# Kernel optimization log

Hardware: AMD Instinct MI355X
Metric: run time of the kernel (lower is better)

Reference implementation:

```python
import jax, jax.numpy as jnp
import numpy as np

B, L, H, N = 8, 8192, 128, 32  # batch, seq_len, d_model, d_state//2 (complex)


def setup_inputs() -> dict:
    key = jax.random.key(0)
    ks = jax.random.split(key, 13)
    x = jax.random.normal(ks[0], (B, L, 2), dtype=jnp.float32)
    enc_w = jax.random.normal(ks[1], (2, H), dtype=jnp.float32) * (1.0 / np.sqrt(2.0))
    enc_b = jax.random.normal(ks[2], (H,), dtype=jnp.float32) * 0.01
    # S4D init: dt log-uniform in [1e-3, 1e-1], A = -0.5 + i*pi*n (S4D-Lin)
    u01 = jax.random.uniform(ks[3], (H,), dtype=jnp.float32)
    log_dt = u01 * (np.log(0.1) - np.log(0.001)) + np.log(0.001)
    log_A_real = jnp.full((H, N), np.log(0.5), dtype=jnp.float32)
    A_imag = jnp.broadcast_to(np.pi * jnp.arange(N, dtype=jnp.float32), (H, N)).copy()
    C_re = jax.random.normal(ks[4], (H, N), dtype=jnp.float32) * (0.5 ** 0.5)
    C_im = jax.random.normal(ks[5], (H, N), dtype=jnp.float32) * (0.5 ** 0.5)
    D = jax.random.normal(ks[6], (H,), dtype=jnp.float32)
    out_w = jax.random.normal(ks[7], (2 * H, H), dtype=jnp.float32) * (1.0 / np.sqrt(H))
    out_b = jax.random.normal(ks[8], (2 * H,), dtype=jnp.float32) * 0.01
    dec_w = jax.random.normal(ks[9], (H, 1), dtype=jnp.float32) * (1.0 / np.sqrt(H))
    dec_b = jax.random.normal(ks[10], (1,), dtype=jnp.float32) * 0.01
    return {"x": x, "enc_w": enc_w, "enc_b": enc_b, "log_dt": log_dt,
            "log_A_real": log_A_real, "A_imag": A_imag, "C_re": C_re,
            "C_im": C_im, "D": D, "out_w": out_w, "out_b": out_b,
            "dec_w": dec_w, "dec_b": dec_b}


def reference(x, enc_w, enc_b, log_dt, log_A_real, A_imag, C_re, C_im, D,
              out_w, out_b, dec_w, dec_b):
    # Encoder (B,L,2) -> (B,L,H), then transpose to channels-first (B,H,L)
    u = jnp.einsum('blc,ch->blh', x, enc_w) + enc_b
    u = jnp.swapaxes(u, -1, -2)  # (B,H,L)
    Lx = u.shape[-1]

    # --- S4D kernel (zero-order-hold discretization, diagonal A) ---
    dt = jnp.exp(log_dt)                      # (H,)
    A = -jnp.exp(log_A_real) + 1j * A_imag    # (H,N) complex
    C = C_re + 1j * C_im                      # (H,N)
    dtA = dt[:, None] * A                     # (H,N)
    K_coef = C * (jnp.exp(dtA) - 1.0) / A     # (H,N)
    # Vandermonde: exp(dtA * l), l = 0..L-1  -> (H,N,L)
    vand = jnp.exp(dtA[:, :, None] * jnp.arange(Lx, dtype=jnp.float32))
    K = 2.0 * jnp.einsum('hn,hnl->hl', K_coef, vand).real  # (H,L)

    # --- causal convolution via FFT (length 2L avoids circular wrap) ---
    n = 2 * Lx
    y = jnp.fft.irfft(jnp.fft.rfft(u, n) * jnp.fft.rfft(K, n), n)[..., :Lx]
    y = y + D[:, None] * u                    # skip connection

    # GELU -> pointwise GLU output projection (Conv1d(H, 2H, 1) + GLU)
    y = jax.nn.gelu(y)
    z = jnp.einsum('bhl,gh->bgl', y, out_w) + out_b[None, :, None]  # (B,2H,L)
    a, g = jnp.split(z, 2, axis=1)
    y = a * jax.nn.sigmoid(g)                 # (B,H,L)

    # Mean-pool over sequence, decode to scalar: (B,1)
    pooled = jnp.mean(y, axis=-1)             # (B,H)
    return pooled @ dec_w + dec_b
```

## Files before the change

### kernel.cpp

```cpp
#include <hip/hip_runtime.h>
#include <math.h>

#define B_ 8
#define L_ 8192
#define H_ 128
#define N_ 32
#define C_ 128
#define T_ 64


typedef _Float16 half8 __attribute__((ext_vector_type(8)));
typedef __attribute__((ext_vector_type(4))) float f32x4;

__device__ __forceinline__ float gelu_tanh(float y) {
    float t = 0.7978845608028654f * fmaf(0.044715f, y * y * y, y);
    float e = __expf(2.f * t);
    float th = 1.f - __fdividef(2.f, e + 1.f);
    return 0.5f * y * (1.f + th);
}
__device__ __forceinline__ unsigned short f2h(float f) {
    _Float16 h = (_Float16)f;
    return *(unsigned short*)&h;
}
__device__ __forceinline__ float h2f(unsigned short u) {
    return (float)(*(const _Float16*)&u);
}

__global__ __launch_bounds__(256) void k_prep(
    const float* __restrict__ log_dt, const float* __restrict__ log_A_real,
    const float* __restrict__ A_imag, const float* __restrict__ C_re,
    const float* __restrict__ C_im, const float* __restrict__ out_w,
    unsigned short* __restrict__ Wh, unsigned short* __restrict__ Kh,
    unsigned short* __restrict__ Ph, unsigned short* __restrict__ Vh)
{
    const int h = blockIdx.x;
    const int tid = threadIdx.x;
    __shared__ float2 wtab[65][N_];
    __shared__ float2 coefs[N_];
    __shared__ float Kd[64];

    float dt = expf(log_dt[h]);
#pragma unroll
    for (int it = 0; it < 9; ++it) {
        int idx = it * 256 + tid;
        if (idx < 65 * N_) {
            int d = idx >> 5, n = idx & 31;
            float Ar = -expf(log_A_real[h * N_ + n]);
            float Ai = A_imag[h * N_ + n];
            float ar = dt * Ar * (float)d, ai = dt * Ai * (float)d;
            float er = expf(ar);
            wtab[d][n] = make_float2(er * cosf(ai), er * sinf(ai));
        }
    }
    if (tid < N_) {
        int n = tid;
        float Ar = -expf(log_A_real[h * N_ + n]);
        float Ai = A_imag[h * N_ + n];
        float ar = dt * Ar, ai = dt * Ai;
        float er = expf(ar);
        float wr = er * cosf(ai), wi = er * sinf(ai);
        float inv = 1.f / (Ar * Ar + Ai * Ai);
        float numr = wr - 1.f, numi = wi;
        float qr = (numr * Ar + numi * Ai) * inv;
        float qi = (numi * Ar - numr * Ai) * inv;
        coefs[n] = make_float2(C_re[h * N_ + n] * qr - C_im[h * N_ + n] * qi,
                               C_re[h * N_ + n] * qi + C_im[h * N_ + n] * qr);
    }
    __syncthreads();
    if (tid < 64) {
        float s = 0.f;
#pragma unroll
        for (int n = 0; n < N_; ++n) {
            float2 cf = coefs[n]; float2 w = wtab[tid][n];
            s += cf.x * w.x - cf.y * w.y;
        }
        Kd[tid] = 2.f * s;
    }
    __syncthreads();
#pragma unroll
    for (int it = 0; it < 16; ++it) {
        int idx = it * 256 + tid;
        int t = idx >> 6, j = idx & 63;
        Kh[h * 4096 + idx] = f2h((t >= j) ? Kd[t - j] : 0.f);
    }
#pragma unroll
    for (int it = 0; it < 16; ++it) {
        int idx = it * 256 + tid;
        int t = idx >> 6, m = idx & 63, n = m & 31;
        float2 cf = coefs[n]; float2 w = wtab[t + 1][n];
        float re = cf.x * w.x - cf.y * w.y;
        float im = cf.x * w.y + cf.y * w.x;
        Ph[h * 4096 + idx] = f2h((m < 32) ? 2.f * re : -2.f * im);
    }
#pragma unroll
    for (int it = 0; it < 16; ++it) {
        int idx = it * 256 + tid;
        int m = idx >> 6, j = idx & 63, n = m & 31;
        float2 w = wtab[63 - j][n];
        Vh[h * 4096 + idx] = f2h((m < 32) ? w.x : w.y);
    }
    {
        int g = 2 * h + (tid >> 7), j = tid & 127;
        Wh[g * 128 + j] = f2h(out_w[g * 128 + j]);
    }
}

__global__ __launch_bounds__(256) void k_s4d(
    const float* __restrict__ x, const float* __restrict__ enc_w,
    const float* __restrict__ enc_b, const float* __restrict__ log_dt,
    const float* __restrict__ log_A_real, const float* __restrict__ A_imag,
    const float* __restrict__ Dp, const unsigned short* __restrict__ Kh,
    const unsigned short* __restrict__ Ph, const unsigned short* __restrict__ Vh,
    unsigned short* __restrict__ gy)
{
    const int bh = blockIdx.x;
    const int b = bh >> 7, h = bh & (H_ - 1);
    const int tid = threadIdx.x;
    const int lane = tid & 63, wq = tid >> 6;
    const int mrow = lane & 15, quad = lane >> 4;

    __shared__ unsigned short Ut[C_][72];
    __shared__ __align__(16) char scratch[18432];
    __shared__ float2 wTpow[7][N_];
    unsigned short* E16 = (unsigned short*)scratch;
    float2*         Sx  = (float2*)scratch;
    unsigned short* St  = (unsigned short*)scratch;

    if (tid < N_) {
        int idx = h * N_ + tid;
        float dt = expf(log_dt[h]);
        float Ar = -expf(log_A_real[idx]);
        float Ai = A_imag[idx];
        float ar = dt * Ar * (float)T_, ai = dt * Ai * (float)T_;
        float er = expf(ar);
        float pr = er * cosf(ai), pi = er * sinf(ai);
#pragma unroll
        for (int k = 0; k < 7; ++k) {
            wTpow[k][tid] = make_float2(pr, pi);
            float nr = pr * pr - pi * pi;
            pi = 2.f * pr * pi; pr = nr;
        }
    }

    const float ew0 = enc_w[h], ew1 = enc_w[H_ + h], eb = enc_b[h];
    {
        int c = tid >> 1, j0 = (tid & 1) * 32;
        const float4* xp = (const float4*)((const float2*)x + (size_t)b * L_
                                           + c * 64 + j0);
#pragma unroll
        for (int i = 0; i < 16; ++i) {
            float4 xv = xp[i];
            float u0 = fmaf(xv.x, ew0, fmaf(xv.y, ew1, eb));
            float u1 = fmaf(xv.z, ew0, fmaf(xv.w, ew1, eb));
            unsigned int pk = (unsigned)f2h(u0) | ((unsigned)f2h(u1) << 16);
            *(unsigned int*)&Ut[c][j0 + 2 * i] = pk;
        }
    }
    __syncthreads();

    {
        f32x4 acc[8];
#pragma unroll
        for (int nt = 0; nt < 8; ++nt) acc[nt] = (f32x4){0.f, 0.f, 0.f, 0.f};
        const unsigned short* Arow = Vh + h * 4096 + (wq * 16 + mrow) * 64;
#pragma unroll
        for (int ks = 0; ks < 2; ++ks) {
            int k0 = ks * 32 + quad * 8;
            half8 af = *(const half8*)(Arow + k0);
#pragma unroll
            for (int nt = 0; nt < 8; ++nt) {
                half8 bf = *(const half8*)&Ut[nt * 16 + mrow][k0];
                acc[nt] = __builtin_amdgcn_mfma_f32_16x16x32_f16(
                    af, bf, acc[nt], 0, 0, 0);
            }
        }
#pragma unroll
        for (int nt = 0; nt < 8; ++nt) {
            int cc = nt * 16 + mrow;
#pragma unroll
            for (int r = 0; r < 4; ++r)
                E16[(wq * 16 + quad * 4 + r) * 136 + cc] = f2h(acc[nt][r]);
        }
    }
    __syncthreads();

    float zr[16], zi[16];
    const int cHalf = wq & 1, nHalf = wq >> 1;
    const int n0 = nHalf * 16;
    const int c = cHalf * 64 + lane;
#pragma unroll
    for (int j = 0; j < 16; ++j) {
        zr[j] = h2f(E16[(n0 + j) * 136 + c]);
        zi[j] = h2f(E16[(32 + n0 + j) * 136 + c]);
    }
    __syncthreads();
#pragma unroll
    for (int k = 0; k < 6; ++k) {
        int s = 1 << k;
        float mask = (lane >= s) ? 1.f : 0.f;
#pragma unroll
        for (int j = 0; j < 16; ++j) {
            float2 q = wTpow[k][n0 + j];
            float vr = __shfl_up(zr[j], s, 64);
            float vi = __shfl_up(zi[j], s, 64);
            float adr = fmaf(q.x, vr, -(q.y * vi));
            float adi = fmaf(q.x, vi, q.y * vr);
            zr[j] = fmaf(mask, adr, zr[j]);
            zi[j] = fmaf(mask, adi, zi[j]);
        }
    }
    if (cHalf == 0) {
#pragma unroll
        for (int j = 0; j < 16; ++j)
            Sx[(n0 + j) * 64 + lane] = make_float2(zr[j], zi[j]);
    }
    __syncthreads();
    if (cHalf == 1) {
#pragma unroll
        for (int j = 0; j < 16; ++j) {
            float2 q = wTpow[6][n0 + j];
            float2 v = Sx[(n0 + j) * 64 + lane];
            zr[j] = fmaf(q.x, v.x, fmaf(-q.y, v.y, zr[j]));
            zi[j] = fmaf(q.x, v.y, fmaf(q.y, v.x, zi[j]));
        }
    }
    {
        bool l0 = (lane == 0);
#pragma unroll
        for (int j = 0; j < 16; ++j) {
            float2 bv = Sx[(n0 + j) * 64 + 63];
            float br = (cHalf == 1) ? bv.x : 0.f;
            float bi = (cHalf == 1) ? bv.y : 0.f;
            float tr = __shfl_up(zr[j], 1, 64);
            float ti = __shfl_up(zi[j], 1, 64);
            zr[j] = l0 ? br : tr;
            zi[j] = l0 ? bi : ti;
        }
    }
    __syncthreads();
    {
#pragma unroll
        for (int j2 = 0; j2 < 8; ++j2) {
            unsigned int p0 = (unsigned)f2h(zr[2 * j2]) |
                              ((unsigned)f2h(zr[2 * j2 + 1]) << 16);
            unsigned int p1 = (unsigned)f2h(zi[2 * j2]) |
                              ((unsigned)f2h(zi[2 * j2 + 1]) << 16);
            *(unsigned int*)&St[c * 72 + n0 + 2 * j2] = p0;
            *(unsigned int*)&St[c * 72 + 32 + n0 + 2 * j2] = p1;
        }
    }
    __syncthreads();

    {
        f32x4 acc[8];
#pragma unroll
        for (int nt = 0; nt < 8; ++nt) acc[nt] = (f32x4){0.f, 0.f, 0.f, 0.f};
        const unsigned short* Krow = Kh + h * 4096 + (wq * 16 + mrow) * 64;
#pragma unroll
        for (int ks = 0; ks < 2; ++ks) {
            int k0 = ks * 32 + quad * 8;
            half8 af = *(const half8*)(Krow + k0);
#pragma unroll
            for (int nt = 0; nt < 8; ++nt) {
                half8 bf = *(const half8*)&Ut[nt * 16 + mrow][k0];
                acc[nt] = __builtin_amdgcn_mfma_f32_16x16x32_f16(
                    af, bf, acc[nt], 0, 0, 0);
            }
        }
        const unsigned short* Prow = Ph + h * 4096 + (wq * 16 + mrow) * 64;
#pragma unroll
        for (int ks = 0; ks < 2; ++ks) {
            int k0 = ks * 32 + quad * 8;
            half8 af = *(const half8*)(Prow + k0);
#pragma unroll
            for (int nt = 0; nt < 8; ++nt) {
                half8 bf = *(const half8*)&St[(nt * 16 + mrow) * 72 + k0];
                acc[nt] = __builtin_amdgcn_mfma_f32_16x16x32_f16(
                    af, bf, acc[nt], 0, 0, 0);
            }
        }
        const float Dh = Dp[h];
        unsigned short* gyb = gy + (size_t)bh * L_;
#pragma unroll
        for (int nt = 0; nt < 8; ++nt) {
            int cc = nt * 16 + mrow;
#pragma unroll
            for (int r = 0; r < 4; ++r) {
                int t = wq * 16 + quad * 4 + r;
                float u = h2f(Ut[cc][t]);
                float y = fmaf(Dh, u, acc[nt][r]);
                gyb[t * 128 + cc] = f2h(gelu_tanh(y));
            }
        }
    }
}

#define BPAD 136
__global__ __launch_bounds__(256) void k_mix(
    const unsigned short* __restrict__ Wh, const unsigned short* __restrict__ gy,
    const float* __restrict__ out_b, const float* __restrict__ dec_w,
    float* __restrict__ part)
{
    __shared__ unsigned short Bt[64 * BPAD];
    __shared__ float red[4];

    const int blk = blockIdx.x;
    const int b = blk >> 7;
    const int t = (blk >> 1) & 63, ch = blk & 1;
    const int tid = threadIdx.x;
    const int wq = tid >> 6, lane = tid & 63;

    const unsigned short* gsrc = gy + (size_t)(b * H_) * L_ + t * 128 + ch * 64;
#pragma unroll
    for (int it = 0; it < 4; ++it) {
        int idx = it * 256 + tid;
        int h = idx >> 3, v0 = (idx & 7) * 8;
        uint4 q = *(const uint4*)(gsrc + (size_t)h * L_ + v0);
        Bt[(v0 + 0) * BPAD + h] = (unsigned short)(q.x & 0xFFFF);
        Bt[(v0 + 1) * BPAD + h] = (unsigned short)(q.x >> 16);
        Bt[(v0 + 2) * BPAD + h] = (unsigned short)(q.y & 0xFFFF);
        Bt[(v0 + 3) * BPAD + h] = (unsigned short)(q.y >> 16);
        Bt[(v0 + 4) * BPAD + h] = (unsigned short)(q.z & 0xFFFF);
        Bt[(v0 + 5) * BPAD + h] = (unsigned short)(q.z >> 16);
        Bt[(v0 + 6) * BPAD + h] = (unsigned short)(q.w & 0xFFFF);
        Bt[(v0 + 7) * BPAD + h] = (unsigned short)(q.w >> 16);
    }
    __syncthreads();

    const int ga = wq * 32;
    const int gg = 128 + wq * 32;
    const int mrow = lane & 15;
    const int quad = lane >> 4;
    f32x4 accA[2][4], accG[2][4];
#pragma unroll
    for (int mt = 0; mt < 2; ++mt)
#pragma unroll
        for (int nt = 0; nt < 4; ++nt) {
            accA[mt][nt] = (f32x4){0.f, 0.f, 0.f, 0.f};
            accG[mt][nt] = (f32x4){0.f, 0.f, 0.f, 0.f};
        }

#pragma unroll
    for (int k = 0; k < 4; ++k) {
        const int h0 = k * 32 + quad * 8;
        half8 bfr[4];
#pragma unroll
        for (int nt = 0; nt < 4; ++nt) {
            int v = nt * 16 + mrow;
            bfr[nt] = *(const half8*)(Bt + v * BPAD + h0);
        }
#pragma unroll
        for (int mt = 0; mt < 2; ++mt) {
            half8 ah = *(const half8*)(Wh + (ga + mt * 16 + mrow) * 128 + h0);
            half8 ag = *(const half8*)(Wh + (gg + mt * 16 + mrow) * 128 + h0);
#pragma unroll
            for (int nt = 0; nt < 4; ++nt) {
                accA[mt][nt] = __builtin_amdgcn_mfma_f32_16x16x32_f16(
                    ah, bfr[nt], accA[mt][nt], 0, 0, 0);
                accG[mt][nt] = __builtin_amdgcn_mfma_f32_16x16x32_f16(
                    ag, bfr[nt], accG[mt][nt], 0, 0, 0);
            }
        }
    }

    float s = 0.f;
#pragma unroll
    for (int mt = 0; mt < 2; ++mt) {
        float4 obA = *(const float4*)(out_b + ga + mt * 16 + quad * 4);
        float4 obG = *(const float4*)(out_b + gg + mt * 16 + quad * 4);
        float4 dv  = *(const float4*)(dec_w + ga + mt * 16 + quad * 4);
#pragma unroll
        for (int nt = 0; nt < 4; ++nt) {
#pragma unroll
            for (int r = 0; r < 4; ++r) {
                float a  = accA[mt][nt][r] + ((const float*)&obA)[r];
                float zg = accG[mt][nt][r] + ((const float*)&obG)[r];
                float sig = __fdividef(1.f, 1.f + __expf(-zg));
                s = fmaf(((const float*)&dv)[r], a * sig, s);
            }
        }
    }
#pragma unroll
    for (int off = 32; off; off >>= 1) s += __shfl_down(s, off, 64);
    if (lane == 0) red[wq] = s;
    __syncthreads();
    if (tid == 0) part[blk] = red[0] + red[1] + red[2] + red[3];
}

__global__ __launch_bounds__(512) void k_final(
    const float* __restrict__ part, const float* __restrict__ dec_b,
    float* __restrict__ out)
{
    int tid = threadIdx.x;
    int b = tid >> 6, lane = tid & 63;
    float s = part[b * 128 + lane] + part[b * 128 + 64 + lane];
#pragma unroll
    for (int off = 32; off; off >>= 1) s += __shfl_down(s, off, 64);
    if (lane == 0) out[b] = fmaf(s, 1.0f / (float)L_, dec_b[0]);
}

extern "C" void kernel_launch(void* const* d_in, const int* in_sizes, int n_in,
                              void* d_out, int out_size, void* d_ws, size_t ws_size,
                              hipStream_t stream)
{
    const float* x         = (const float*)d_in[0];
    const float* enc_w     = (const float*)d_in[1];
    const float* enc_b     = (const float*)d_in[2];
    const float* log_dt    = (const float*)d_in[3];
    const float* log_A_real= (const float*)d_in[4];
    const float* A_imag    = (const float*)d_in[5];
    const float* C_re      = (const float*)d_in[6];
    const float* C_im      = (const float*)d_in[7];
    const float* Dp        = (const float*)d_in[8];
    const float* out_w     = (const float*)d_in[9];
    const float* out_b     = (const float*)d_in[10];
    const float* dec_w     = (const float*)d_in[11];
    const float* dec_b     = (const float*)d_in[12];
    float* out = (float*)d_out;

    char* ws = (char*)d_ws;
    unsigned short* Wh = (unsigned short*)(ws);
    unsigned short* Kh = (unsigned short*)(ws + 65536);
    unsigned short* Ph = (unsigned short*)(ws + 1114112);
    unsigned short* Vh = (unsigned short*)(ws + 2162688);
    unsigned short* gy = (unsigned short*)(ws + 3211264);
    float* part        = (float*)(ws + 19988480);

    k_prep<<<H_, 256, 0, stream>>>(log_dt, log_A_real, A_imag, C_re, C_im,
                                   out_w, Wh, Kh, Ph, Vh);
    k_s4d<<<B_ * H_, 256, 0, stream>>>(x, enc_w, enc_b, log_dt, log_A_real,
                                       A_imag, Dp, Kh, Ph, Vh, gy);
    k_mix<<<B_ * 128, 256, 0, stream>>>(Wh, gy, out_b, dec_w, part);
    k_final<<<1, 512, 0, stream>>>(part, dec_b, out);
}
```

Measured before the change: 141.1 us.

## Fuse S4D operator-matrix prep into main kernel, computing K/P/V tiles on the fly

Removes the separate k_prep launch and its global Kh/Ph/Vh fp16 matrices. The conv-kernel taps, the state-projection matrix and the Vandermonde matrix are now computed per block in registers with fast exp and sincos, and the K taps go through shared memory. This drops a kernel launch and the global round trip for those matrices. In exchange each of the B*H blocks repeats the per-channel transcendental work, and the fast intrinsics may lose some accuracy. The Wh conversion is done by the b==0 blocks, which still finish before k_mix runs.

```diff
diff --git a/kernel.cpp b/kernel.cpp
--- a/kernel.cpp
+++ b/kernel.cpp
@@ -26,36 +26,37 @@
     return (float)(*(const _Float16*)&u);
 }
 
-__global__ __launch_bounds__(256) void k_prep(
-    const float* __restrict__ log_dt, const float* __restrict__ log_A_real,
-    const float* __restrict__ A_imag, const float* __restrict__ C_re,
-    const float* __restrict__ C_im, const float* __restrict__ out_w,
-    unsigned short* __restrict__ Wh, unsigned short* __restrict__ Kh,
-    unsigned short* __restrict__ Ph, unsigned short* __restrict__ Vh)
+__global__ __launch_bounds__(256) void k_s4d(
+    const float* __restrict__ x, const float* __restrict__ enc_w,
+    const float* __restrict__ enc_b, const float* __restrict__ log_dt,
+    const float* __restrict__ log_A_real, const float* __restrict__ A_imag,
+    const float* __restrict__ C_re, const float* __restrict__ C_im,
+    const float* __restrict__ Dp, const float* __restrict__ out_w,
+    unsigned short* __restrict__ Wh, unsigned short* __restrict__ gy)
 {
-    const int h = blockIdx.x;
+    const int bh = blockIdx.x;
+    const int b = bh >> 7, h = bh & (H_ - 1);
     const int tid = threadIdx.x;
-    __shared__ float2 wtab[65][N_];
+    const int lane = tid & 63, wq = tid >> 6;
+    const int mrow = lane & 15, quad = lane >> 4;
+
+    __shared__ unsigned short Ut[C_][72];
+    __shared__ __align__(16) char scratch[18432];
+    __shared__ float2 wTpow[7][N_];
     __shared__ float2 coefs[N_];
-    __shared__ float Kd[64];
-
-    float dt = expf(log_dt[h]);
-#pragma unroll
-    for (int it = 0; it < 9; ++it) {
-        int idx = it * 256 + tid;
-        if (idx < 65 * N_) {
-            int d = idx >> 5, n = idx & 31;
-            float Ar = -expf(log_A_real[h * N_ + n]);
-            float Ai = A_imag[h * N_ + n];
-            float ar = dt * Ar * (float)d, ai = dt * Ai * (float)d;
-            float er = expf(ar);
-            wtab[d][n] = make_float2(er * cosf(ai), er * sinf(ai));
-        }
-    }
+    __shared__ float2 ArAi[N_];
+    __shared__ float  Kd[64];
+    unsigned short* E16 = (unsigned short*)scratch;
+    float2*         Sx  = (float2*)scratch;
+    unsigned short* St  = (unsigned short*)scratch;
+
+    const float dt = expf(log_dt[h]);
+
     if (tid < N_) {
         int n = tid;
         float Ar = -expf(log_A_real[h * N_ + n]);
         float Ai = A_imag[h * N_ + n];
+        ArAi[n] = make_float2(Ar, Ai);
         float ar = dt * Ar, ai = dt * Ai;
         float er = expf(ar);
         float wr = er * cosf(ai), wi = er * sinf(ai);
@@ -65,81 +66,20 @@
         float qi = (numi * Ar - numr * Ai) * inv;
         coefs[n] = make_float2(C_re[h * N_ + n] * qr - C_im[h * N_ + n] * qi,
                                C_re[h * N_ + n] * qi + C_im[h * N_ + n] * qr);
-    }
-    __syncthreads();
-    if (tid < 64) {
-        float s = 0.f;
-#pragma unroll
-        for (int n = 0; n < N_; ++n) {
-            float2 cf = coefs[n]; float2 w = wtab[tid][n];
-            s += cf.x * w.x - cf.y * w.y;
-        }
-        Kd[tid] = 2.f * s;
-    }
-    __syncthreads();
-#pragma unroll
-    for (int it = 0; it < 16; ++it) {
-        int idx = it * 256 + tid;
-        int t = idx >> 6, j = idx & 63;
-        Kh[h * 4096 + idx] = f2h((t >= j) ? Kd[t - j] : 0.f);
-    }
-#pragma unroll
-    for (int it = 0; it < 16; ++it) {
-        int idx = it * 256 + tid;
-        int t = idx >> 6, m = idx & 63, n = m & 31;
-        float2 cf = coefs[n]; float2 w = wtab[t + 1][n];
-        float re = cf.x * w.x - cf.y * w.y;
-        float im = cf.x * w.y + cf.y * w.x;
-        Ph[h * 4096 + idx] = f2h((m < 32) ? 2.f * re : -2.f * im);
-    }
-#pragma unroll
-    for (int it = 0; it < 16; ++it) {
-        int idx = it * 256 + tid;
-        int m = idx >> 6, j = idx & 63, n = m & 31;
-        float2 w = wtab[63 - j][n];
-        Vh[h * 4096 + idx] = f2h((m < 32) ? w.x : w.y);
-    }
-    {
+        float arT = dt * Ar * (float)T_, aiT = dt * Ai * (float)T_;
+        float erT = expf(arT);
+        float pr = erT * cosf(aiT), pi = erT * sinf(aiT);
+#pragma unroll
+        for (int k = 0; k < 7; ++k) {
+            wTpow[k][n] = make_float2(pr, pi);
+            float nr = pr * pr - pi * pi;
+            pi = 2.f * pr * pi; pr = nr;
+        }
+    }
+
+    if (b == 0) {
         int g = 2 * h + (tid >> 7), j = tid & 127;
         Wh[g * 128 + j] = f2h(out_w[g * 128 + j]);
-    }
-}
-
-__global__ __launch_bounds__(256) void k_s4d(
-    const float* __restrict__ x, const float* __restrict__ enc_w,
-    const float* __restrict__ enc_b, const float* __restrict__ log_dt,
-    const float* __restrict__ log_A_real, const float* __restrict__ A_imag,
-    const float* __restrict__ Dp, const unsigned short* __restrict__ Kh,
-    const unsigned short* __restrict__ Ph, const unsigned short* __restrict__ Vh,
-    unsigned short* __restrict__ gy)
-{
-    const int bh = blockIdx.x;
-    const int b = bh >> 7, h = bh & (H_ - 1);
-    const int tid = threadIdx.x;
-    const int lane = tid & 63, wq = tid >> 6;
-    const int mrow = lane & 15, quad = lane >> 4;
-
-    __shared__ unsigned short Ut[C_][72];
-    __shared__ __align__(16) char scratch[18432];
-    __shared__ float2 wTpow[7][N_];
-    unsigned short* E16 = (unsigned short*)scratch;
-    float2*         Sx  = (float2*)scratch;
-    unsigned short* St  = (unsigned short*)scratch;
-
-    if (tid < N_) {
-        int idx = h * N_ + tid;
-        float dt = expf(log_dt[h]);
-        float Ar = -expf(log_A_real[idx]);
-        float Ai = A_imag[idx];
-        float ar = dt * Ar * (float)T_, ai = dt * Ai * (float)T_;
-        float er = expf(ar);
-        float pr = er * cosf(ai), pi = er * sinf(ai);
-#pragma unroll
-        for (int k = 0; k < 7; ++k) {
-            wTpow[k][tid] = make_float2(pr, pi);
-            float nr = pr * pr - pi * pi;
-            pi = 2.f * pr * pi; pr = nr;
-        }
     }
 
     const float ew0 = enc_w[h], ew1 = enc_w[H_ + h], eb = enc_b[h];
@@ -159,14 +99,40 @@
     __syncthreads();
 
     {
+        int t = tid >> 2, q = tid & 3;
+        float s = 0.f;
+        float ft = (float)t;
+#pragma unroll
+        for (int k = 0; k < 8; ++k) {
+            int n = q * 8 + k;
+            float2 cf = coefs[n]; float2 aa = ArAi[n];
+            float er = __expf(dt * aa.x * ft);
+            float sn, cs; __sincosf(dt * aa.y * ft, &sn, &cs);
+            s = fmaf(cf.x, er * cs, s);
+            s = fmaf(-cf.y, er * sn, s);
+        }
+        ((float*)&Ut[t][64])[q] = s;
+    }
+
+    {
         f32x4 acc[8];
 #pragma unroll
         for (int nt = 0; nt < 8; ++nt) acc[nt] = (f32x4){0.f, 0.f, 0.f, 0.f};
-        const unsigned short* Arow = Vh + h * 4096 + (wq * 16 + mrow) * 64;
+        const int m = wq * 16 + mrow;
+        const float2 aa = ArAi[m & 31];
+        const float dAr = dt * aa.x, dAi = dt * aa.y;
+        const bool isIm = (m >= 32);
 #pragma unroll
         for (int ks = 0; ks < 2; ++ks) {
             int k0 = ks * 32 + quad * 8;
-            half8 af = *(const half8*)(Arow + k0);
+            half8 af;
+#pragma unroll
+            for (int i = 0; i < 8; ++i) {
+                float d = (float)(63 - (k0 + i));
+                float er = __expf(dAr * d);
+                float sn, cs; __sincosf(dAi * d, &sn, &cs);
+                af[i] = (_Float16)(isIm ? er * sn : er * cs);
+            }
 #pragma unroll
             for (int nt = 0; nt < 8; ++nt) {
                 half8 bf = *(const half8*)&Ut[nt * 16 + mrow][k0];
@@ -183,6 +149,11 @@
         }
     }
     __syncthreads();
+
+    if (tid < 64) {
+        const float* kp = (const float*)&Ut[tid][64];
+        Kd[tid] = 2.f * (kp[0] + kp[1] + kp[2] + kp[3]);
+    }
 
     float zr[16], zi[16];
     const int cHalf = wq & 1, nHalf = wq >> 1;
@@ -255,11 +226,16 @@
         f32x4 acc[8];
 #pragma unroll
         for (int nt = 0; nt < 8; ++nt) acc[nt] = (f32x4){0.f, 0.f, 0.f, 0.f};
-        const unsigned short* Krow = Kh + h * 4096 + (wq * 16 + mrow) * 64;
+        const int t = wq * 16 + mrow;
 #pragma unroll
         for (int ks = 0; ks < 2; ++ks) {
             int k0 = ks * 32 + quad * 8;
-            half8 af = *(const half8*)(Krow + k0);
+            half8 af;
+#pragma unroll
+            for (int i = 0; i < 8; ++i) {
+                int j = k0 + i;
+                af[i] = (_Float16)((t >= j) ? Kd[t - j] : 0.f);
+            }
 #pragma unroll
             for (int nt = 0; nt < 8; ++nt) {
                 half8 bf = *(const half8*)&Ut[nt * 16 + mrow][k0];
@@ -267,11 +243,24 @@
                     af, bf, acc[nt], 0, 0, 0);
             }
         }
-        const unsigned short* Prow = Ph + h * 4096 + (wq * 16 + mrow) * 64;
+        half8 afP0, afP1;
+        {
+            float tp1 = (float)(t + 1);
+#pragma unroll
+            for (int i = 0; i < 8; ++i) {
+                int n = quad * 8 + i;
+                float2 cf = coefs[n]; float2 aa = ArAi[n];
+                float er = __expf(dt * aa.x * tp1);
+                float sn, cs; __sincosf(dt * aa.y * tp1, &sn, &cs);
+                float wr = er * cs, wi = er * sn;
+                afP0[i] = (_Float16)( 2.f * (cf.x * wr - cf.y * wi));
+                afP1[i] = (_Float16)(-2.f * (cf.x * wi + cf.y * wr));
+            }
+        }
 #pragma unroll
         for (int ks = 0; ks < 2; ++ks) {
             int k0 = ks * 32 + quad * 8;
-            half8 af = *(const half8*)(Prow + k0);
+            half8 af = ks ? afP1 : afP0;
 #pragma unroll
             for (int nt = 0; nt < 8; ++nt) {
                 half8 bf = *(const half8*)&St[(nt * 16 + mrow) * 72 + k0];
@@ -286,10 +275,10 @@
             int cc = nt * 16 + mrow;
 #pragma unroll
             for (int r = 0; r < 4; ++r) {
-                int t = wq * 16 + quad * 4 + r;
-                float u = h2f(Ut[cc][t]);
+                int tt = wq * 16 + quad * 4 + r;
+                float u = h2f(Ut[cc][tt]);
                 float y = fmaf(Dh, u, acc[nt][r]);
-                gyb[t * 128 + cc] = f2h(gelu_tanh(y));
+                gyb[tt * 128 + cc] = f2h(gelu_tanh(y));
             }
         }
     }
@@ -420,16 +409,11 @@
 
     char* ws = (char*)d_ws;
     unsigned short* Wh = (unsigned short*)(ws);
-    unsigned short* Kh = (unsigned short*)(ws + 65536);
-    unsigned short* Ph = (unsigned short*)(ws + 1114112);
-    unsigned short* Vh = (unsigned short*)(ws + 2162688);
     unsigned short* gy = (unsigned short*)(ws + 3211264);
     float* part        = (float*)(ws + 19988480);
 
-    k_prep<<<H_, 256, 0, stream>>>(log_dt, log_A_real, A_imag, C_re, C_im,
-                                   out_w, Wh, Kh, Ph, Vh);
     k_s4d<<<B_ * H_, 256, 0, stream>>>(x, enc_w, enc_b, log_dt, log_A_real,
-                                       A_imag, Dp, Kh, Ph, Vh, gy);
+                                       A_imag, C_re, C_im, Dp, out_w, Wh, gy);
     k_mix<<<B_ * 128, 256, 0, stream>>>(Wh, gy, out_b, dec_w, part);
     k_final<<<1, 512, 0, stream>>>(part, dec_b, out);
 }
```

Measured after the change: 132.5 us. 6.1% less time.
